# Performance work log

Hardware: AMD Instinct MI355X
Metric: run time of the kernel (lower is better)

Reference implementation:

```python
import jax, jax.numpy as jnp
import numpy as np

D_MODEL = 1024
N_HEADS = 16
N_GROUPS = 4
D_HEAD = D_MODEL // N_HEADS  # 64
HPG = N_HEADS // N_GROUPS    # heads per KV group = 4
B, T = 2, 2048


def _rope(x):
    # x: [B, H, T, D]; interleaved even/odd rotary, matching the torch module
    t, d = x.shape[2], x.shape[3]
    pos = jnp.arange(t, dtype=jnp.float32)[:, None]                      # [T,1]
    freq = jnp.exp(-(jnp.arange(0, d, 2, dtype=jnp.float32) / d)
                   * jnp.log(jnp.float32(10000.0)))                      # [D/2]
    angle = pos * freq                                                   # [T, D/2]
    cos, sin = jnp.cos(angle), jnp.sin(angle)
    xe, xo = x[..., ::2], x[..., 1::2]
    re = xe * cos - xo * sin
    ro = xe * sin + xo * cos
    return jnp.stack([re, ro], axis=-1).reshape(x.shape)


def setup_inputs() -> dict:
    key = jax.random.key(0)
    ks = jax.random.split(key, 10)
    s = 0.02
    return {
        "x":  jax.random.normal(ks[0], (B, T, D_MODEL), dtype=jnp.float32),
        "Wq": jax.random.normal(ks[1], (D_MODEL, D_MODEL), dtype=jnp.float32) * s,
        "bq": jax.random.normal(ks[2], (D_MODEL,), dtype=jnp.float32) * s,
        "Wk": jax.random.normal(ks[3], (D_MODEL, N_GROUPS * D_HEAD), dtype=jnp.float32) * s,
        "bk": jax.random.normal(ks[4], (N_GROUPS * D_HEAD,), dtype=jnp.float32) * s,
        "Wv": jax.random.normal(ks[5], (D_MODEL, N_GROUPS * D_HEAD), dtype=jnp.float32) * s,
        "bv": jax.random.normal(ks[6], (N_GROUPS * D_HEAD,), dtype=jnp.float32) * s,
        "Wo": jax.random.normal(ks[7], (D_MODEL, D_MODEL), dtype=jnp.float32) * s,
        "bo": jax.random.normal(ks[8], (D_MODEL,), dtype=jnp.float32) * s,
    }


def reference(x, Wq, bq, Wk, bk, Wv, bv, Wo, bo):
    b, t, _ = x.shape
    q = (x @ Wq + bq).reshape(b, t, N_HEADS, D_HEAD).transpose(0, 2, 1, 3)    # [B,H,T,D]
    k = (x @ Wk + bk).reshape(b, t, N_GROUPS, D_HEAD).transpose(0, 2, 1, 3)   # [B,G,T,D]
    v = (x @ Wv + bv).reshape(b, t, N_GROUPS, D_HEAD).transpose(0, 2, 1, 3)
    # GQA broadcast: idx = arange(n_heads) // heads_per_group  ==  repeat each group HPG times
    k = jnp.repeat(k, HPG, axis=1)                                            # [B,H,T,D]
    v = jnp.repeat(v, HPG, axis=1)
    q = _rope(q)
    k = _rope(k)
    scale = jnp.float32(np.sqrt(D_HEAD))
    scores = jnp.einsum('bhtd,bhsd->bhts', q, k) / scale                      # [B,H,T,T]
    causal = jnp.tril(jnp.ones((t, t), dtype=bool))
    scores = jnp.where(causal, scores, -jnp.inf)
    probs = jax.nn.softmax(scores, axis=-1)
    # dropout(p=0.05) is identity in eval mode
    attn = jnp.einsum('bhts,bhsd->bhtd', probs, v)
    out = attn.transpose(0, 2, 1, 3).reshape(b, t, N_HEADS * D_HEAD)
    return out @ Wo + bo
```

## Files before the change

kernel.cpp:

```cpp
#include <hip/hip_runtime.h>
#include <stdint.h>

typedef unsigned short u16;
typedef __attribute__((ext_vector_type(4))) float f32x4;
typedef __attribute__((ext_vector_type(8))) short bf16x8;
typedef __attribute__((ext_vector_type(4))) short bf16x4;

#define T_SEQ 2048
#define DM 1024
#define NH 16
#define NG 4
#define DH 64
#define QSCALE 0.18033688011112042f

__device__ __forceinline__ u16 f2bf(float f) {
    union { float f; uint32_t u; } v; v.f = f;
    uint32_t r = (v.u + 0x7FFFu + ((v.u >> 16) & 1u)) >> 16;
    return (u16)r;
}
__device__ __forceinline__ float bf2f(u16 u) {
    union { uint32_t u; float f; } v; v.u = ((uint32_t)u) << 16;
    return v.f;
}
__device__ __forceinline__ float fexp2(float x) {
#if __has_builtin(__builtin_amdgcn_exp2f)
    return __builtin_amdgcn_exp2f(x);
#else
    return exp2f(x);
#endif
}
__device__ __forceinline__ uint32_t cvtpk_bf16(float a, float b) {
    uint32_t r;
    asm("v_cvt_pk_bf16_f32 %0, %1, %2" : "=v"(r) : "v"(a), "v"(b));
    return r;
}

#if __has_builtin(__builtin_amdgcn_mfma_f32_16x16x16_bf16)
__device__ __forceinline__ f32x4 mfma16(bf16x4 a, bf16x4 b, f32x4 c) {
    return __builtin_amdgcn_mfma_f32_16x16x16_bf16(a, b, c, 0, 0, 0);
}
#elif __has_builtin(__builtin_amdgcn_mfma_f32_16x16x16bf16_1k)
__device__ __forceinline__ f32x4 mfma16(bf16x4 a, bf16x4 b, f32x4 c) {
    return __builtin_amdgcn_mfma_f32_16x16x16bf16_1k(a, b, c, 0, 0, 0);
}
#else
__device__ __forceinline__ f32x4 mfma16(bf16x4 a, bf16x4 b, f32x4 c) {
    asm("v_mfma_f32_16x16x16_bf16 %0, %1, %2, %0" : "+v"(c) : "v"(a), "v"(b));
    return c;
}
#endif

__device__ __forceinline__ void async16(const void* g, void* l) {
    __builtin_amdgcn_global_load_lds(
        (const __attribute__((address_space(1))) void*)g,
        (__attribute__((address_space(3))) void*)l,
        16, 0, 0);
}

__global__ __launch_bounds__(256) void k_prep(
    const float* __restrict__ x, u16* __restrict__ xb,
    const float* __restrict__ Wq, const float* __restrict__ Wk,
    const float* __restrict__ Wv, const float* __restrict__ Wo,
    u16* __restrict__ wqkvt, u16* __restrict__ wot,
    const float* __restrict__ bq, const float* __restrict__ bk,
    const float* __restrict__ bv, float* __restrict__ bqkv,
    float2* __restrict__ tbl) {
    int blk = blockIdx.x;
    int tid = threadIdx.x;
    if (blk < 2048) {
        int i = blk * 256 + tid;
        const float4* p = (const float4*)x + (size_t)i * 2;
        float4 a = p[0], b = p[1];
        bf16x8 v;
        v[0] = (short)f2bf(a.x); v[1] = (short)f2bf(a.y);
        v[2] = (short)f2bf(a.z); v[3] = (short)f2bf(a.w);
        v[4] = (short)f2bf(b.x); v[5] = (short)f2bf(b.y);
        v[6] = (short)f2bf(b.z); v[7] = (short)f2bf(b.w);
        ((bf16x8*)xb)[i] = v;
        return;
    }
    int t = blk - 2048;
    if (t >= 2560) {
        int u = t - 2560;
        if (u < 6) {
            int i = u * 256 + tid;
            if (i < 1536) {
                float v;
                if (i < 1024) v = bq[i];
                else if (i < 1280) v = bk[i - 1024];
                else v = bv[i - 1280];
                bqkv[i] = v;
            }
        } else {
            int idx = (u - 6) * 256 + tid;
            int tt = idx >> 5, i = idx & 31;
            float freq = exp2f(-(float)i * (13.287712379549449f / 32.0f));
            float ang = (float)tt * freq;
            tbl[idx] = make_float2(cosf(ang), sinf(ang));
        }
        return;
    }
    const float* src; u16* dst; int N;
    if (t < 1024)      { src = Wq; dst = wqkvt;                      N = 1024; }
    else if (t < 1280) { t -= 1024; src = Wk; dst = wqkvt + (size_t)1024 * 1024; N = 256; }
    else if (t < 1536) { t -= 1280; src = Wv; dst = wqkvt + (size_t)1280 * 1024; N = 256; }
    else               { t -= 1536; src = Wo; dst = wot;             N = 1024; }
    int ntiles = N >> 5;
    int n0 = (t % ntiles) * 32, k0 = (t / ntiles) * 32;
    __shared__ float tile[32][33];
    int tx = tid & 31, ty = tid >> 5;
#pragma unroll
    for (int q = 0; q < 4; q++)
        tile[ty + q * 8][tx] = src[(size_t)(k0 + ty + q * 8) * N + n0 + tx];
    __syncthreads();
#pragma unroll
    for (int q = 0; q < 4; q++)
        dst[(size_t)(n0 + ty + q * 8) * 1024 + k0 + tx] = f2bf(tile[tx][ty + q * 8]);
}

template <int EPI>
__global__ __launch_bounds__(256) void k_gemm(
    const u16* __restrict__ A, const u16* __restrict__ Bt,
    const float* __restrict__ bias, float* __restrict__ C,
    const float2* __restrict__ tbl, u16* __restrict__ Qo,
    u16* __restrict__ Ko, u16* __restrict__ Vto, int N, int K) {
    __shared__ __align__(16) u16 As[2][64 * 64];
    __shared__ __align__(16) u16 Bs[2][128 * 64];
    int tid = threadIdx.x;
    int lane = tid & 63, wid = tid >> 6;
    int wr = wid >> 1, wc = wid & 1;
    int l15 = lane & 15, lhi = lane >> 4;
    int row0 = blockIdx.y * 64, col0 = blockIdx.x * 128;
    f32x4 acc[2][4] = {};

    const u16* ga[2];
    const u16* gb[4];
#pragma unroll
    for (int i = 0; i < 2; i++) {
        int c = i * 256 + tid, r = c >> 3, sch = (c & 7) ^ (r & 7);
        ga[i] = A + (size_t)(row0 + r) * K + sch * 8;
    }
#pragma unroll
    for (int i = 0; i < 4; i++) {
        int c = i * 256 + tid, r = c >> 3, sch = (c & 7) ^ (r & 7);
        gb[i] = Bt + (size_t)(col0 + r) * K + sch * 8;
    }

#pragma unroll
    for (int i = 0; i < 2; i++) async16(ga[i], &As[0][(i * 256 + tid) * 8]);
#pragma unroll
    for (int i = 0; i < 4; i++) async16(gb[i], &Bs[0][(i * 256 + tid) * 8]);
    __syncthreads();

    int nk = K >> 6;
    for (int kt = 0; kt < nk; kt++) {
        int cur = kt & 1;
        if (kt + 1 < nk) {
            int nx = cur ^ 1, ko = (kt + 1) << 6;
#pragma unroll
            for (int i = 0; i < 2; i++) async16(ga[i] + ko, &As[nx][(i * 256 + tid) * 8]);
#pragma unroll
            for (int i = 0; i < 4; i++) async16(gb[i] + ko, &Bs[nx][(i * 256 + tid) * 8]);
        }
        const u16* Ac = As[cur];
        const u16* Bc = Bs[cur];
#pragma unroll
        for (int ks = 0; ks < 2; ks++) {
            bf16x8 af[2], bfr[4];
#pragma unroll
            for (int m = 0; m < 2; m++) {
                int r = wr * 32 + m * 16 + l15;
                int kb = (ks * 64 + lhi * 16) ^ ((r & 7) << 4);
                af[m] = *(const bf16x8*)((const char*)Ac + r * 128 + kb);
            }
#pragma unroll
            for (int n = 0; n < 4; n++) {
                int r = wc * 64 + n * 16 + l15;
                int kb = (ks * 64 + lhi * 16) ^ ((r & 7) << 4);
                bfr[n] = *(const bf16x8*)((const char*)Bc + r * 128 + kb);
            }
#pragma unroll
            for (int m = 0; m < 2; m++)
#pragma unroll
                for (int n = 0; n < 4; n++)
                    acc[m][n] = __builtin_amdgcn_mfma_f32_16x16x32_bf16(
                        af[m], bfr[n], acc[m][n], 0, 0, 0);
        }
        __syncthreads();
    }

    if (EPI == 0) {
#pragma unroll
        for (int n = 0; n < 4; n++) {
            int col = col0 + wc * 64 + n * 16 + l15;
            float bv = bias[col];
#pragma unroll
            for (int m = 0; m < 2; m++) {
                int row = row0 + wr * 32 + m * 16 + lhi * 4;
#pragma unroll
                for (int i = 0; i < 4; i++)
                    C[(size_t)(row + i) * N + col] = acc[m][n][i] + bv;
            }
        }
    } else {
        int type = (col0 >= 1280) ? 2 : (col0 >= 1024 ? 1 : 0);
        int rbase = row0 + wr * 32;
#pragma unroll
        for (int n = 0; n < 4; n++) {
            int col = col0 + wc * 64 + n * 16 + l15;
            float bv = bias[col];
            if (type == 2) {
                int cc = col - 1280;
                int g = cc >> 6, d = cc & 63;
#pragma unroll
                for (int m = 0; m < 2; m++)
#pragma unroll
                    for (int i = 0; i < 4; i++) {
                        int rowg = rbase + m * 16 + lhi * 4 + i;
                        int t = rowg & (T_SEQ - 1), b = rowg >> 11;
                        int sp = t ^ ((d & 1) << 2);
                        Vto[(((size_t)(b * NG + g)) * DH + d) * T_SEQ + sp] =
                            f2bf(acc[m][n][i] + bv);
                    }
            } else {
                float ssgn = (col & 1) ? 1.f : -1.f;
                int ip = (col & 63) >> 1;
#pragma unroll
                for (int m = 0; m < 2; m++)
#pragma unroll
                    for (int i = 0; i < 4; i++) {
                        int rowg = rbase + m * 16 + lhi * 4 + i;
                        int t = rowg & (T_SEQ - 1), b = rowg >> 11;
                        float v = acc[m][n][i] + bv;
                        float other = __shfl_xor(v, 1);
                        float2 cs = tbl[t * 32 + ip];
                        float out = v * cs.x + other * cs.y * ssgn;
                        if (type == 0) {
                            int h = col >> 6, d = col & 63;
                            Qo[(((size_t)(b * NH + h)) * T_SEQ + t) * DH + d] =
                                f2bf(out * QSCALE);
                        } else {
                            int cc = col - 1024;
                            int g = cc >> 6, d = cc & 63;
                            Ko[(((size_t)(b * NG + g)) * T_SEQ + t) * DH + d] = f2bf(out);
                        }
                    }
            }
        }
    }
}

__global__ __launch_bounds__(256) void k_attn(
    const u16* __restrict__ Q, const u16* __restrict__ K,
    const u16* __restrict__ Vt, u16* __restrict__ Aout) {
    int i0 = blockIdx.x;
    int u = i0 >> 5;
    int qt = (u < 16) ? (31 - u) : (u - 16);
    int bh = i0 & 31;
    int b = bh >> 4, h = bh & 15, g = h >> 2;
    int tid = threadIdx.x;
    int lane = tid & 63, wid = tid >> 6;
    int l15 = lane & 15, lhi = lane >> 4;

    const u16* Kp = K + ((size_t)(b * NG + g)) * T_SEQ * DH;
    const u16* Vp = Vt + ((size_t)(b * NG + g)) * DH * T_SEQ;

    __shared__ __align__(16) u16 Ks[2][64 * 64];
    __shared__ __align__(16) u16 Vs[3][64 * 64];

    const u16* Qp = Q + ((size_t)bh * T_SEQ + qt * 64) * DH;
    bf16x8 qf[2];
#pragma unroll
    for (int ks = 0; ks < 2; ks++)
        qf[ks] = *(const bf16x8*)(Qp + (size_t)(wid * 16 + l15) * DH + ks * 32 + lhi * 8);

    f32x4 of[4] = {};
    float m_i = -3.0e38f, l_i = 0.f;

    int nt = qt + 1;
    int swz = (l15 & 7) << 4;

    int c0 = tid, c1 = tid + 256;
    int rk0 = c0 >> 3, rk1 = c1 >> 3;
    int sk0 = (c0 & 7) ^ (rk0 & 7);
    int sk1 = (c1 & 7) ^ (rk1 & 7);
    int sv0 = (c0 & 7) ^ ((rk0 >> 1) & 7);
    int sv1 = (c1 & 7) ^ ((rk1 >> 1) & 7);
    const u16* kg0 = Kp + rk0 * DH + sk0 * 8;
    const u16* kg1 = Kp + rk1 * DH + sk1 * 8;
    const u16* vg0 = Vp + (size_t)rk0 * T_SEQ + sv0 * 8;
    const u16* vg1 = Vp + (size_t)rk1 * T_SEQ + sv1 * 8;

    async16(kg0, &Ks[0][c0 * 8]);
    async16(kg1, &Ks[0][c1 * 8]);
    async16(vg0, &Vs[0][c0 * 8]);
    async16(vg1, &Vs[0][c1 * 8]);
    __syncthreads();
    if (nt > 1) {
        async16(kg0 + (1 << 12), &Ks[1][c0 * 8]);
        async16(kg1 + (1 << 12), &Ks[1][c1 * 8]);
        async16(vg0 + (1 << 6), &Vs[1][c0 * 8]);
        async16(vg1 + (1 << 6), &Vs[1][c1 * 8]);
    }
    f32x4 sf[4] = {};
    __builtin_amdgcn_s_setprio(1);
#pragma unroll
    for (int ks = 0; ks < 2; ks++)
#pragma unroll
        for (int n = 0; n < 4; n++) {
            int kb = (ks * 64 + lhi * 16) ^ swz;
            bf16x8 kf = *(const bf16x8*)((const char*)Ks[0] + (n * 16 + l15) * 128 + kb);
            sf[n] = __builtin_amdgcn_mfma_f32_16x16x32_bf16(kf, qf[ks], sf[n], 0, 0, 0);
        }
    __builtin_amdgcn_s_setprio(0);
    __syncthreads();

    u16* vread = Vs[0];
    u16* vhold = Vs[1];
    u16* vstage = Vs[2];

#pragma unroll 1
    for (int it = 1; it < nt; it++) {
        if (it + 1 < nt) {
            int ko = (it + 1) << 12, vo = (it + 1) << 6;
            int nx = (it + 1) & 1;
            async16(kg0 + ko, &Ks[nx][c0 * 8]);
            async16(kg1 + ko, &Ks[nx][c1 * 8]);
            async16(vg0 + vo, vstage + c0 * 8);
            async16(vg1 + vo, vstage + c1 * 8);
        }

        float pmt = sf[0][0];
#pragma unroll
        for (int n = 0; n < 4; n++)
#pragma unroll
            for (int i = 0; i < 4; i++)
                pmt = fmaxf(pmt, sf[n][i]);
        if (!__all(pmt - m_i <= 8.f)) {
#pragma unroll
            for (int off = 16; off <= 32; off <<= 1)
                pmt = fmaxf(pmt, __shfl_xor(pmt, off));
            float mn = fmaxf(m_i, pmt);
            float sc = fexp2(m_i - mn);
            m_i = mn;
            l_i *= sc;
            float sc4[4];
#pragma unroll
            for (int i = 0; i < 4; i++)
                sc4[i] = __shfl(sc, lhi * 4 + i);
#pragma unroll
            for (int n = 0; n < 4; n++)
#pragma unroll
                for (int i = 0; i < 4; i++)
                    of[n][i] *= sc4[i];
        }
        bf16x4 pa[4];
#pragma unroll
        for (int n = 0; n < 4; n++) {
#pragma unroll
            for (int i = 0; i < 4; i++) {
                float p = fexp2(sf[n][i] - m_i);
                sf[n][i] = p;
                l_i += p;
            }
            union { uint32_t uu[2]; bf16x4 v; } pu;
            pu.uu[0] = cvtpk_bf16(sf[n][0], sf[n][1]);
            pu.uu[1] = cvtpk_bf16(sf[n][2], sf[n][3]);
            pa[n] = pu.v;
        }

        const u16* Kc = Ks[it & 1];
        __builtin_amdgcn_s_setprio(1);
#pragma unroll
        for (int ks = 0; ks < 2; ks++)
#pragma unroll
            for (int n = 0; n < 4; n++) {
                int kb = (ks * 64 + lhi * 16) ^ swz;
                bf16x8 kf = *(const bf16x8*)((const char*)Kc + (n * 16 + l15) * 128 + kb);
                f32x4 z = (ks == 0) ? f32x4{0.f, 0.f, 0.f, 0.f} : sf[n];
                sf[n] = __builtin_amdgcn_mfma_f32_16x16x32_bf16(kf, qf[ks], z, 0, 0, 0);
            }

#pragma unroll
        for (int nd = 0; nd < 4; nd++) {
            int rowb = (nd * 16 + l15) * 128;
#pragma unroll
            for (int n = 0; n < 4; n++) {
                int kb = ((4 * n + lhi) ^ l15) << 3;
                bf16x4 vf = *(const bf16x4*)((const char*)vread + rowb + kb);
                of[nd] = mfma16(pa[n], vf, of[nd]);
            }
        }
        __builtin_amdgcn_s_setprio(0);

        u16* tmp = vread; vread = vhold; vhold = vstage; vstage = tmp;
        __syncthreads();
    }

    {
        int qrow = qt * 64 + wid * 16 + l15;
        int sb = (nt - 1) * 64 + lhi * 4;
#pragma unroll
        for (int n = 0; n < 4; n++)
#pragma unroll
            for (int i = 0; i < 4; i++)
                if (sb + n * 16 + i > qrow) sf[n][i] = -3.0e38f;
        float pmt = sf[0][0];
#pragma unroll
        for (int n = 0; n < 4; n++)
#pragma unroll
            for (int i = 0; i < 4; i++)
                pmt = fmaxf(pmt, sf[n][i]);
        if (!__all(pmt - m_i <= 8.f)) {
#pragma unroll
            for (int off = 16; off <= 32; off <<= 1)
                pmt = fmaxf(pmt, __shfl_xor(pmt, off));
            float mn = fmaxf(m_i, pmt);
            float sc = fexp2(m_i - mn);
            m_i = mn;
            l_i *= sc;
            float sc4[4];
#pragma unroll
            for (int i = 0; i < 4; i++)
                sc4[i] = __shfl(sc, lhi * 4 + i);
#pragma unroll
            for (int n = 0; n < 4; n++)
#pragma unroll
                for (int i = 0; i < 4; i++)
                    of[n][i] *= sc4[i];
        }
        bf16x4 pa[4];
#pragma unroll
        for (int n = 0; n < 4; n++) {
#pragma unroll
            for (int i = 0; i < 4; i++) {
                float p = fexp2(sf[n][i] - m_i);
                sf[n][i] = p;
                l_i += p;
            }
            union { uint32_t uu[2]; bf16x4 v; } pu;
            pu.uu[0] = cvtpk_bf16(sf[n][0], sf[n][1]);
            pu.uu[1] = cvtpk_bf16(sf[n][2], sf[n][3]);
            pa[n] = pu.v;
        }
        __builtin_amdgcn_s_setprio(1);
#pragma unroll
        for (int nd = 0; nd < 4; nd++) {
            int rowb = (nd * 16 + l15) * 128;
#pragma unroll
            for (int n = 0; n < 4; n++) {
                int kb = ((4 * n + lhi) ^ l15) << 3;
                bf16x4 vf = *(const bf16x4*)((const char*)vread + rowb + kb);
                of[nd] = mfma16(pa[n], vf, of[nd]);
            }
        }
        __builtin_amdgcn_s_setprio(0);
    }

#pragma unroll
    for (int off = 16; off <= 32; off <<= 1)
        l_i += __shfl_xor(l_i, off);
    float lq[4];
#pragma unroll
    for (int i = 0; i < 4; i++)
        lq[i] = __shfl(l_i, lhi * 4 + i);
#pragma unroll
    for (int n = 0; n < 4; n++)
#pragma unroll
        for (int i = 0; i < 4; i++) {
            int trow = qt * 64 + wid * 16 + lhi * 4 + i;
            float v = of[n][i] / lq[i];
            Aout[((size_t)(b * T_SEQ + trow)) * DM + h * 64 + n * 16 + l15] = f2bf(v);
        }
}

extern "C" void kernel_launch(void* const* d_in, const int* in_sizes, int n_in,
                              void* d_out, int out_size, void* d_ws, size_t ws_size,
                              hipStream_t stream) {
    const float* x  = (const float*)d_in[0];
    const float* Wq = (const float*)d_in[1];
    const float* bq = (const float*)d_in[2];
    const float* Wk = (const float*)d_in[3];
    const float* bk = (const float*)d_in[4];
    const float* Wv = (const float*)d_in[5];
    const float* bv = (const float*)d_in[6];
    const float* Wo = (const float*)d_in[7];
    const float* bo = (const float*)d_in[8];

    char* ws = (char*)d_ws;
    size_t o = 0;
    u16*   xb    = (u16*)(ws + o);  o += (size_t)4096 * 1024 * 2;
    u16*   wqkvt = (u16*)(ws + o);  o += (size_t)1536 * 1024 * 2;
    u16*   wot   = (u16*)(ws + o);  o += (size_t)1024 * 1024 * 2;
    float* bqkv  = (float*)(ws + o); o += 1536 * 4;
    o = (o + 255) & ~(size_t)255;
    u16*   Qb    = (u16*)(ws + o);  o += (size_t)2 * NH * T_SEQ * DH * 2;
    u16*   Kb    = (u16*)(ws + o);  o += (size_t)2 * NG * T_SEQ * DH * 2;
    u16*   Vtb   = (u16*)(ws + o);  o += (size_t)2 * NG * DH * T_SEQ * 2;
    u16*   attnb = (u16*)(ws + o);  o += (size_t)4096 * 1024 * 2;
    float2* tbl  = (float2*)(ws + o); o += (size_t)2048 * 32 * 8;

    k_prep<<<4870, 256, 0, stream>>>(x, xb, Wq, Wk, Wv, Wo, wqkvt, wot, bq, bk, bv, bqkv, tbl);
    k_gemm<1><<<dim3(12, 64), 256, 0, stream>>>(xb, wqkvt, bqkv, nullptr, tbl, Qb, Kb, Vtb, 1536, 1024);
    k_attn<<<1024, 256, 0, stream>>>(Qb, Kb, Vtb, attnb);
    k_gemm<0><<<dim3(8, 64), 256, 0, stream>>>(attnb, wot, bo, (float*)d_out, nullptr, nullptr, nullptr, nullptr, 1024, 1024);
}
```

Baseline: 88.58 us.

## Shrink GEMM column tiles and fold running max into attention score accumulator

The GEMM kernels get a template parameter for the column tile width. The QKV projection now uses 96-wide tiles and the output projection 64-wide tiles, which raises block counts to fill more CUs at the cost of less B-operand reuse. In attention, the running max is subtracted by seeding the QK MFMA accumulator with -m_i, so the common no-rescale path computes exp2 directly without a subtract. The 16-way max reduction also uses v_max3. This adds a duplicated exp path, and it changes initial m_i to 0, which relies on the threshold logic staying numerically safe.

Result: slower. 91.41 us (+3.2%).

```diff
diff --git a/kernel.cpp b/kernel.cpp
--- a/kernel.cpp
+++ b/kernel.cpp
@@ -32,6 +32,11 @@
 __device__ __forceinline__ uint32_t cvtpk_bf16(float a, float b) {
     uint32_t r;
     asm("v_cvt_pk_bf16_f32 %0, %1, %2" : "=v"(r) : "v"(a), "v"(b));
+    return r;
+}
+__device__ __forceinline__ float max3f(float a, float b, float c) {
+    float r;
+    asm("v_max3_f32 %0, %1, %2, %3" : "=v"(r) : "v"(a), "v"(b), "v"(c));
     return r;
 }
 
@@ -118,30 +123,30 @@
         dst[(size_t)(n0 + ty + q * 8) * 1024 + k0 + tx] = f2bf(tile[tx][ty + q * 8]);
 }
 
-template <int EPI>
+template <int EPI, int NB>
 __global__ __launch_bounds__(256) void k_gemm(
     const u16* __restrict__ A, const u16* __restrict__ Bt,
     const float* __restrict__ bias, float* __restrict__ C,
     const float2* __restrict__ tbl, u16* __restrict__ Qo,
     u16* __restrict__ Ko, u16* __restrict__ Vto, int N, int K) {
     __shared__ __align__(16) u16 As[2][64 * 64];
-    __shared__ __align__(16) u16 Bs[2][128 * 64];
+    __shared__ __align__(16) u16 Bs[2][NB * 32 * 64];
     int tid = threadIdx.x;
     int lane = tid & 63, wid = tid >> 6;
     int wr = wid >> 1, wc = wid & 1;
     int l15 = lane & 15, lhi = lane >> 4;
-    int row0 = blockIdx.y * 64, col0 = blockIdx.x * 128;
-    f32x4 acc[2][4] = {};
+    int row0 = blockIdx.y * 64, col0 = blockIdx.x * (NB * 32);
+    f32x4 acc[2][NB] = {};
 
     const u16* ga[2];
-    const u16* gb[4];
+    const u16* gb[NB];
 #pragma unroll
     for (int i = 0; i < 2; i++) {
         int c = i * 256 + tid, r = c >> 3, sch = (c & 7) ^ (r & 7);
         ga[i] = A + (size_t)(row0 + r) * K + sch * 8;
     }
 #pragma unroll
-    for (int i = 0; i < 4; i++) {
+    for (int i = 0; i < NB; i++) {
         int c = i * 256 + tid, r = c >> 3, sch = (c & 7) ^ (r & 7);
         gb[i] = Bt + (size_t)(col0 + r) * K + sch * 8;
     }
@@ -149,7 +154,7 @@
 #pragma unroll
     for (int i = 0; i < 2; i++) async16(ga[i], &As[0][(i * 256 + tid) * 8]);
 #pragma unroll
-    for (int i = 0; i < 4; i++) async16(gb[i], &Bs[0][(i * 256 + tid) * 8]);
+    for (int i = 0; i < NB; i++) async16(gb[i], &Bs[0][(i * 256 + tid) * 8]);
     __syncthreads();
 
     int nk = K >> 6;
@@ -160,13 +165,13 @@
 #pragma unroll
             for (int i = 0; i < 2; i++) async16(ga[i] + ko, &As[nx][(i * 256 + tid) * 8]);
 #pragma unroll
-            for (int i = 0; i < 4; i++) async16(gb[i] + ko, &Bs[nx][(i * 256 + tid) * 8]);
+            for (int i = 0; i < NB; i++) async16(gb[i] + ko, &Bs[nx][(i * 256 + tid) * 8]);
         }
         const u16* Ac = As[cur];
         const u16* Bc = Bs[cur];
 #pragma unroll
         for (int ks = 0; ks < 2; ks++) {
-            bf16x8 af[2], bfr[4];
+            bf16x8 af[2], bfr[NB];
 #pragma unroll
             for (int m = 0; m < 2; m++) {
                 int r = wr * 32 + m * 16 + l15;
@@ -174,78 +179,70 @@
                 af[m] = *(const bf16x8*)((const char*)Ac + r * 128 + kb);
             }
 #pragma unroll
-            for (int n = 0; n < 4; n++) {
-                int r = wc * 64 + n * 16 + l15;
+            for (int n = 0; n < NB; n++) {
+                int r = wc * (NB * 16) + n * 16 + l15;
                 int kb = (ks * 64 + lhi * 16) ^ ((r & 7) << 4);
                 bfr[n] = *(const bf16x8*)((const char*)Bc + r * 128 + kb);
             }
 #pragma unroll
             for (int m = 0; m < 2; m++)
 #pragma unroll
-                for (int n = 0; n < 4; n++)
+                for (int n = 0; n < NB; n++)
                     acc[m][n] = __builtin_amdgcn_mfma_f32_16x16x32_bf16(
                         af[m], bfr[n], acc[m][n], 0, 0, 0);
         }
         __syncthreads();
     }
 
-    if (EPI == 0) {
-#pragma unroll
-        for (int n = 0; n < 4; n++) {
-            int col = col0 + wc * 64 + n * 16 + l15;
-            float bv = bias[col];
+    int rbase = row0 + wr * 32;
+#pragma unroll
+    for (int n = 0; n < NB; n++) {
+        int col = col0 + wc * (NB * 16) + n * 16 + l15;
+        float bv = bias[col];
+        if (EPI == 0) {
 #pragma unroll
             for (int m = 0; m < 2; m++) {
-                int row = row0 + wr * 32 + m * 16 + lhi * 4;
+                int row = rbase + m * 16 + lhi * 4;
 #pragma unroll
                 for (int i = 0; i < 4; i++)
                     C[(size_t)(row + i) * N + col] = acc[m][n][i] + bv;
             }
-        }
-    } else {
-        int type = (col0 >= 1280) ? 2 : (col0 >= 1024 ? 1 : 0);
-        int rbase = row0 + wr * 32;
-#pragma unroll
-        for (int n = 0; n < 4; n++) {
-            int col = col0 + wc * 64 + n * 16 + l15;
-            float bv = bias[col];
-            if (type == 2) {
-                int cc = col - 1280;
-                int g = cc >> 6, d = cc & 63;
-#pragma unroll
-                for (int m = 0; m < 2; m++)
-#pragma unroll
-                    for (int i = 0; i < 4; i++) {
-                        int rowg = rbase + m * 16 + lhi * 4 + i;
-                        int t = rowg & (T_SEQ - 1), b = rowg >> 11;
-                        int sp = t ^ ((d & 1) << 2);
-                        Vto[(((size_t)(b * NG + g)) * DH + d) * T_SEQ + sp] =
-                            f2bf(acc[m][n][i] + bv);
+        } else if (col >= 1280) {
+            int cc = col - 1280;
+            int g = cc >> 6, d = cc & 63;
+#pragma unroll
+            for (int m = 0; m < 2; m++)
+#pragma unroll
+                for (int i = 0; i < 4; i++) {
+                    int rowg = rbase + m * 16 + lhi * 4 + i;
+                    int t = rowg & (T_SEQ - 1), b = rowg >> 11;
+                    int sp = t ^ ((d & 1) << 2);
+                    Vto[(((size_t)(b * NG + g)) * DH + d) * T_SEQ + sp] =
+                        f2bf(acc[m][n][i] + bv);
+                }
+        } else {
+            float ssgn = (col & 1) ? 1.f : -1.f;
+            int ip = (col & 63) >> 1;
+#pragma unroll
+            for (int m = 0; m < 2; m++)
+#pragma unroll
+                for (int i = 0; i < 4; i++) {
+                    int rowg = rbase + m * 16 + lhi * 4 + i;
+                    int t = rowg & (T_SEQ - 1), b = rowg >> 11;
+                    float v = acc[m][n][i] + bv;
+                    float other = __shfl_xor(v, 1);
+                    float2 cs = tbl[t * 32 + ip];
+                    float out = v * cs.x + other * cs.y * ssgn;
+                    if (col < 1024) {
+                        int h = col >> 6, d = col & 63;
+                        Qo[(((size_t)(b * NH + h)) * T_SEQ + t) * DH + d] =
+                            f2bf(out * QSCALE);
+                    } else {
+                        int cc = col - 1024;
+                        int g = cc >> 6, d = cc & 63;
+                        Ko[(((size_t)(b * NG + g)) * T_SEQ + t) * DH + d] = f2bf(out);
                     }
-            } else {
-                float ssgn = (col & 1) ? 1.f : -1.f;
-                int ip = (col & 63) >> 1;
-#pragma unroll
-                for (int m = 0; m < 2; m++)
-#pragma unroll
-                    for (int i = 0; i < 4; i++) {
-                        int rowg = rbase + m * 16 + lhi * 4 + i;
-                        int t = rowg & (T_SEQ - 1), b = rowg >> 11;
-                        float v = acc[m][n][i] + bv;
-                        float other = __shfl_xor(v, 1);
-                        float2 cs = tbl[t * 32 + ip];
-                        float out = v * cs.x + other * cs.y * ssgn;
-                        if (type == 0) {
-                            int h = col >> 6, d = col & 63;
-                            Qo[(((size_t)(b * NH + h)) * T_SEQ + t) * DH + d] =
-                                f2bf(out * QSCALE);
-                        } else {
-                            int cc = col - 1024;
-                            int g = cc >> 6, d = cc & 63;
-                            Ko[(((size_t)(b * NG + g)) * T_SEQ + t) * DH + d] = f2bf(out);
-                        }
-                    }
-            }
+                }
         }
     }
 }
@@ -275,7 +272,7 @@
         qf[ks] = *(const bf16x8*)(Qp + (size_t)(wid * 16 + l15) * DH + ks * 32 + lhi * 8);
 
     f32x4 of[4] = {};
-    float m_i = -3.0e38f, l_i = 0.f;
+    float m_i = 0.f, l_i = 0.f;
 
     int nt = qt + 1;
     int swz = (l15 & 7) << 4;
@@ -330,19 +327,20 @@
             async16(vg1 + vo, vstage + c1 * 8);
         }
 
-        float pmt = sf[0][0];
-#pragma unroll
-        for (int n = 0; n < 4; n++)
-#pragma unroll
-            for (int i = 0; i < 4; i++)
-                pmt = fmaxf(pmt, sf[n][i]);
-        if (!__all(pmt - m_i <= 8.f)) {
+        float t0 = max3f(sf[0][0], sf[0][1], sf[0][2]);
+        float t1 = max3f(sf[0][3], sf[1][0], sf[1][1]);
+        float t2 = max3f(sf[1][2], sf[1][3], sf[2][0]);
+        float t3 = max3f(sf[2][1], sf[2][2], sf[2][3]);
+        float t4 = max3f(sf[3][0], sf[3][1], sf[3][2]);
+        float pmt = fmaxf(max3f(t0, t1, t2), max3f(t3, t4, sf[3][3]));
+        bf16x4 pa[4];
+        if (!__all(pmt <= 8.f)) {
 #pragma unroll
             for (int off = 16; off <= 32; off <<= 1)
                 pmt = fmaxf(pmt, __shfl_xor(pmt, off));
-            float mn = fmaxf(m_i, pmt);
-            float sc = fexp2(m_i - mn);
-            m_i = mn;
+            float dm = fmaxf(pmt, 0.f);
+            m_i += dm;
+            float sc = fexp2(-dm);
             l_i *= sc;
             float sc4[4];
 #pragma unroll
@@ -353,22 +351,36 @@
 #pragma unroll
                 for (int i = 0; i < 4; i++)
                     of[n][i] *= sc4[i];
-        }
-        bf16x4 pa[4];
-#pragma unroll
-        for (int n = 0; n < 4; n++) {
-#pragma unroll
-            for (int i = 0; i < 4; i++) {
-                float p = fexp2(sf[n][i] - m_i);
-                sf[n][i] = p;
-                l_i += p;
-            }
-            union { uint32_t uu[2]; bf16x4 v; } pu;
-            pu.uu[0] = cvtpk_bf16(sf[n][0], sf[n][1]);
-            pu.uu[1] = cvtpk_bf16(sf[n][2], sf[n][3]);
-            pa[n] = pu.v;
-        }
-
+#pragma unroll
+            for (int n = 0; n < 4; n++) {
+#pragma unroll
+                for (int i = 0; i < 4; i++) {
+                    float p = fexp2(sf[n][i] - dm);
+                    sf[n][i] = p;
+                    l_i += p;
+                }
+                union { uint32_t uu[2]; bf16x4 v; } pu;
+                pu.uu[0] = cvtpk_bf16(sf[n][0], sf[n][1]);
+                pu.uu[1] = cvtpk_bf16(sf[n][2], sf[n][3]);
+                pa[n] = pu.v;
+            }
+        } else {
+#pragma unroll
+            for (int n = 0; n < 4; n++) {
+#pragma unroll
+                for (int i = 0; i < 4; i++) {
+                    float p = fexp2(sf[n][i]);
+                    sf[n][i] = p;
+                    l_i += p;
+                }
+                union { uint32_t uu[2]; bf16x4 v; } pu;
+                pu.uu[0] = cvtpk_bf16(sf[n][0], sf[n][1]);
+                pu.uu[1] = cvtpk_bf16(sf[n][2], sf[n][3]);
+                pa[n] = pu.v;
+            }
+        }
+
+        float nm = -m_i;
         const u16* Kc = Ks[it & 1];
         __builtin_amdgcn_s_setprio(1);
 #pragma unroll
@@ -377,7 +389,7 @@
             for (int n = 0; n < 4; n++) {
                 int kb = (ks * 64 + lhi * 16) ^ swz;
                 bf16x8 kf = *(const bf16x8*)((const char*)Kc + (n * 16 + l15) * 128 + kb);
-                f32x4 z = (ks == 0) ? f32x4{0.f, 0.f, 0.f, 0.f} : sf[n];
+                f32x4 z = (ks == 0) ? f32x4{nm, nm, nm, nm} : sf[n];
                 sf[n] = __builtin_amdgcn_mfma_f32_16x16x32_bf16(kf, qf[ks], z, 0, 0, 0);
             }
 
@@ -405,19 +417,19 @@
 #pragma unroll
             for (int i = 0; i < 4; i++)
                 if (sb + n * 16 + i > qrow) sf[n][i] = -3.0e38f;
-        float pmt = sf[0][0];
-#pragma unroll
-        for (int n = 0; n < 4; n++)
-#pragma unroll
-            for (int i = 0; i < 4; i++)
-                pmt = fmaxf(pmt, sf[n][i]);
-        if (!__all(pmt - m_i <= 8.f)) {
+        float t0 = max3f(sf[0][0], sf[0][1], sf[0][2]);
+        float t1 = max3f(sf[0][3], sf[1][0], sf[1][1]);
+        float t2 = max3f(sf[1][2], sf[1][3], sf[2][0]);
+        float t3 = max3f(sf[2][1], sf[2][2], sf[2][3]);
+        float t4 = max3f(sf[3][0], sf[3][1], sf[3][2]);
+        float pmt = fmaxf(max3f(t0, t1, t2), max3f(t3, t4, sf[3][3]));
+        bf16x4 pa[4];
+        if (!__all(pmt <= 8.f)) {
 #pragma unroll
             for (int off = 16; off <= 32; off <<= 1)
                 pmt = fmaxf(pmt, __shfl_xor(pmt, off));
-            float mn = fmaxf(m_i, pmt);
-            float sc = fexp2(m_i - mn);
-            m_i = mn;
+            float dm = fmaxf(pmt, 0.f);
+            float sc = fexp2(-dm);
             l_i *= sc;
             float sc4[4];
 #pragma unroll
@@ -428,20 +440,33 @@
 #pragma unroll
                 for (int i = 0; i < 4; i++)
                     of[n][i] *= sc4[i];
-        }
-        bf16x4 pa[4];
-#pragma unroll
-        for (int n = 0; n < 4; n++) {
-#pragma unroll
-            for (int i = 0; i < 4; i++) {
-                float p = fexp2(sf[n][i] - m_i);
-                sf[n][i] = p;
-                l_i += p;
-            }
-            union { uint32_t uu[2]; bf16x4 v; } pu;
-            pu.uu[0] = cvtpk_bf16(sf[n][0], sf[n][1]);
-            pu.uu[1] = cvtpk_bf16(sf[n][2], sf[n][3]);
-            pa[n] = pu.v;
+#pragma unroll
+            for (int n = 0; n < 4; n++) {
+#pragma unroll
+                for (int i = 0; i < 4; i++) {
+                    float p = fexp2(sf[n][i] - dm);
+                    sf[n][i] = p;
+                    l_i += p;
+                }
+                union { uint32_t uu[2]; bf16x4 v; } pu;
+                pu.uu[0] = cvtpk_bf16(sf[n][0], sf[n][1]);
+                pu.uu[1] = cvtpk_bf16(sf[n][2], sf[n][3]);
+                pa[n] = pu.v;
+            }
+        } else {
+#pragma unroll
+            for (int n = 0; n < 4; n++) {
+#pragma unroll
+                for (int i = 0; i < 4; i++) {
+                    float p = fexp2(sf[n][i]);
+                    sf[n][i] = p;
+                    l_i += p;
+                }
+                union { uint32_t uu[2]; bf16x4 v; } pu;
+                pu.uu[0] = cvtpk_bf16(sf[n][0], sf[n][1]);
+                pu.uu[1] = cvtpk_bf16(sf[n][2], sf[n][3]);
+                pa[n] = pu.v;
+            }
         }
         __builtin_amdgcn_s_setprio(1);
 #pragma unroll
@@ -501,7 +526,7 @@
     float2* tbl  = (float2*)(ws + o); o += (size_t)2048 * 32 * 8;
 
     k_prep<<<4870, 256, 0, stream>>>(x, xb, Wq, Wk, Wv, Wo, wqkvt, wot, bq, bk, bv, bqkv, tbl);
-    k_gemm<1><<<dim3(12, 64), 256, 0, stream>>>(xb, wqkvt, bqkv, nullptr, tbl, Qb, Kb, Vtb, 1536, 1024);
+    k_gemm<1, 3><<<dim3(16, 64), 256, 0, stream>>>(xb, wqkvt, bqkv, nullptr, tbl, Qb, Kb, Vtb, 1536, 1024);
     k_attn<<<1024, 256, 0, stream>>>(Qb, Kb, Vtb, attnb);
-    k_gemm<0><<<dim3(8, 64), 256, 0, stream>>>(attnb, wot, bo, (float*)d_out, nullptr, nullptr, nullptr, nullptr, 1024, 1024);
-}
+    k_gemm<0, 2><<<dim3(16, 64), 256, 0, stream>>>(attnb, wot, bo, (float*)d_out, nullptr, nullptr, nullptr, nullptr, 1024, 1024);
+}
```

## Split long causal query tiles across two blocks with a combine kernel

Applied to the files above, without the earlier changes.

Query tiles 16-31, which carry the most causal KV work, are each split into two blocks that cover halves of the KV range. The halves write unnormalized partial outputs plus row max and sum to workspace, and a new combine kernel merges them with a log-sum-exp rescale. A constant task table interleaves split and unsplit work to even out load across the 1536 blocks. The goal is to shorten the critical path of the longest blocks, at the cost of an extra kernel launch and fp32 partial-output traffic.

Result: slower. 92.25 us (+4.1%).

```diff
diff --git a/kernel.cpp b/kernel.cpp
--- a/kernel.cpp
+++ b/kernel.cpp
@@ -56,6 +56,15 @@
         (__attribute__((address_space(3))) void*)l,
         16, 0, 0);
 }
+
+__constant__ unsigned char d_task_qt[48] = {
+    31,31,30,15,30,29,29,28,14,28,27,27,26,13,26,25,25,24,12,24,
+    23,23,22,11,22,21,21,20,10,20,19,19,18, 9,18,17,17,16, 8,16,
+     7, 6, 5, 4, 3, 2, 1, 0};
+__constant__ unsigned char d_task_sh[48] = {
+    2,3,2,0,3,2,3,2,0,3,2,3,2,0,3,2,3,2,0,3,
+    2,3,2,0,3,2,3,2,0,3,2,3,2,0,3,2,3,2,0,3,
+    0,0,0,0,0,0,0,0};
 
 __global__ __launch_bounds__(256) void k_prep(
     const float* __restrict__ x, u16* __restrict__ xb,
@@ -252,11 +261,19 @@
 
 __global__ __launch_bounds__(256) void k_attn(
     const u16* __restrict__ Q, const u16* __restrict__ K,
-    const u16* __restrict__ Vt, u16* __restrict__ Aout) {
-    int i0 = blockIdx.x;
-    int u = i0 >> 5;
-    int qt = (u < 16) ? (31 - u) : (u - 16);
-    int bh = i0 & 31;
+    const u16* __restrict__ Vt, u16* __restrict__ Aout,
+    float* __restrict__ Opart, float* __restrict__ mlbuf) {
+    int w = blockIdx.x >> 5;
+    int bh = blockIdx.x & 31;
+    int qt = d_task_qt[w];
+    int sh = d_task_sh[w];
+    int split = sh >> 1, half = sh & 1;
+    int hmid = (qt + 2) >> 1;
+    int t0 = (split && half) ? hmid : 0;
+    int t1 = split ? (half ? qt + 1 : hmid) : qt + 1;
+    int nt = t1 - t0;
+    int diag = (t1 == qt + 1);
+
     int b = bh >> 4, h = bh & 15, g = h >> 2;
     int tid = threadIdx.x;
     int lane = tid & 63, wid = tid >> 6;
@@ -276,8 +293,6 @@
 
     f32x4 of[4] = {};
     float m_i = -3.0e38f, l_i = 0.f;
-
-    int nt = qt + 1;
     int swz = (l15 & 7) << 4;
 
     int c0 = tid, c1 = tid + 256;
@@ -291,16 +306,20 @@
     const u16* vg0 = Vp + (size_t)rk0 * T_SEQ + sv0 * 8;
     const u16* vg1 = Vp + (size_t)rk1 * T_SEQ + sv1 * 8;
 
-    async16(kg0, &Ks[0][c0 * 8]);
-    async16(kg1, &Ks[0][c1 * 8]);
-    async16(vg0, &Vs[0][c0 * 8]);
-    async16(vg1, &Vs[0][c1 * 8]);
+    {
+        int ko = t0 << 12, vo = t0 << 6;
+        async16(kg0 + ko, &Ks[0][c0 * 8]);
+        async16(kg1 + ko, &Ks[0][c1 * 8]);
+        async16(vg0 + vo, &Vs[0][c0 * 8]);
+        async16(vg1 + vo, &Vs[0][c1 * 8]);
+    }
     __syncthreads();
     if (nt > 1) {
-        async16(kg0 + (1 << 12), &Ks[1][c0 * 8]);
-        async16(kg1 + (1 << 12), &Ks[1][c1 * 8]);
-        async16(vg0 + (1 << 6), &Vs[1][c0 * 8]);
-        async16(vg1 + (1 << 6), &Vs[1][c1 * 8]);
+        int ko = (t0 + 1) << 12, vo = (t0 + 1) << 6;
+        async16(kg0 + ko, &Ks[1][c0 * 8]);
+        async16(kg1 + ko, &Ks[1][c1 * 8]);
+        async16(vg0 + vo, &Vs[1][c0 * 8]);
+        async16(vg1 + vo, &Vs[1][c1 * 8]);
     }
     f32x4 sf[4] = {};
     __builtin_amdgcn_s_setprio(1);
@@ -322,7 +341,7 @@
 #pragma unroll 1
     for (int it = 1; it < nt; it++) {
         if (it + 1 < nt) {
-            int ko = (it + 1) << 12, vo = (it + 1) << 6;
+            int ko = (t0 + it + 1) << 12, vo = (t0 + it + 1) << 6;
             int nx = (it + 1) & 1;
             async16(kg0 + ko, &Ks[nx][c0 * 8]);
             async16(kg1 + ko, &Ks[nx][c1 * 8]);
@@ -398,13 +417,15 @@
     }
 
     {
-        int qrow = qt * 64 + wid * 16 + l15;
-        int sb = (nt - 1) * 64 + lhi * 4;
-#pragma unroll
-        for (int n = 0; n < 4; n++)
-#pragma unroll
-            for (int i = 0; i < 4; i++)
-                if (sb + n * 16 + i > qrow) sf[n][i] = -3.0e38f;
+        if (diag) {
+            int qrow = qt * 64 + wid * 16 + l15;
+            int sb = (t1 - 1) * 64 + lhi * 4;
+#pragma unroll
+            for (int n = 0; n < 4; n++)
+#pragma unroll
+                for (int i = 0; i < 4; i++)
+                    if (sb + n * 16 + i > qrow) sf[n][i] = -3.0e38f;
+        }
         float pmt = sf[0][0];
 #pragma unroll
         for (int n = 0; n < 4; n++)
@@ -460,18 +481,68 @@
 #pragma unroll
     for (int off = 16; off <= 32; off <<= 1)
         l_i += __shfl_xor(l_i, off);
-    float lq[4];
-#pragma unroll
-    for (int i = 0; i < 4; i++)
-        lq[i] = __shfl(l_i, lhi * 4 + i);
-#pragma unroll
-    for (int n = 0; n < 4; n++)
-#pragma unroll
-        for (int i = 0; i < 4; i++) {
-            int trow = qt * 64 + wid * 16 + lhi * 4 + i;
-            float v = of[n][i] / lq[i];
-            Aout[((size_t)(b * T_SEQ + trow)) * DM + h * 64 + n * 16 + l15] = f2bf(v);
-        }
+
+    if (split) {
+        int tileix = (qt - 16) * 32 + bh;
+        float* Op = Opart + ((size_t)tileix * 2 + half) * 4096;
+#pragma unroll
+        for (int n = 0; n < 4; n++)
+#pragma unroll
+            for (int i = 0; i < 4; i++)
+                Op[(wid * 16 + lhi * 4 + i) * 64 + n * 16 + l15] = of[n][i];
+        if (lhi == 0) {
+            int base = tileix * 256 + half * 128;
+            mlbuf[base + wid * 16 + l15] = m_i;
+            mlbuf[base + 64 + wid * 16 + l15] = l_i;
+        }
+    } else {
+        float lq[4];
+#pragma unroll
+        for (int i = 0; i < 4; i++)
+            lq[i] = __shfl(l_i, lhi * 4 + i);
+#pragma unroll
+        for (int n = 0; n < 4; n++)
+#pragma unroll
+            for (int i = 0; i < 4; i++) {
+                int trow = qt * 64 + wid * 16 + lhi * 4 + i;
+                float v = of[n][i] / lq[i];
+                Aout[((size_t)(b * T_SEQ + trow)) * DM + h * 64 + n * 16 + l15] = f2bf(v);
+            }
+    }
+}
+
+__global__ __launch_bounds__(256) void k_combine(
+    const float* __restrict__ Opart, const float* __restrict__ mlbuf,
+    u16* __restrict__ Aout) {
+    int j = blockIdx.x;
+    int qt = 16 + (j >> 5), bh = j & 31;
+    int b = bh >> 4, h = bh & 15;
+    int tid = threadIdx.x;
+    int lane = tid & 63, wid = tid >> 6;
+    int l15 = lane & 15, lhi = lane >> 4;
+
+    const float* OA = Opart + (size_t)j * 2 * 4096;
+    const float* OB = OA + 4096;
+    int mb = j * 256;
+
+#pragma unroll
+    for (int i = 0; i < 4; i++) {
+        int r = wid * 16 + lhi * 4 + i;
+        float mA = mlbuf[mb + r];
+        float lA = mlbuf[mb + 64 + r];
+        float mB = mlbuf[mb + 128 + r];
+        float lB = mlbuf[mb + 192 + r];
+        float M = fmaxf(mA, mB);
+        float sA = fexp2(mA - M), sB = fexp2(mB - M);
+        float linv = 1.f / (lA * sA + lB * sB);
+        int trow = qt * 64 + r;
+#pragma unroll
+        for (int n = 0; n < 4; n++) {
+            int d = n * 16 + l15;
+            float v = (OA[r * 64 + d] * sA + OB[r * 64 + d] * sB) * linv;
+            Aout[((size_t)(b * T_SEQ + trow)) * DM + h * 64 + d] = f2bf(v);
+        }
+    }
 }
 
 extern "C" void kernel_launch(void* const* d_in, const int* in_sizes, int n_in,
@@ -499,9 +570,12 @@
     u16*   Vtb   = (u16*)(ws + o);  o += (size_t)2 * NG * DH * T_SEQ * 2;
     u16*   attnb = (u16*)(ws + o);  o += (size_t)4096 * 1024 * 2;
     float2* tbl  = (float2*)(ws + o); o += (size_t)2048 * 32 * 8;
+    float* Opart = (float*)(ws + o); o += (size_t)512 * 2 * 4096 * 4;
+    float* mlbuf = (float*)(ws + o); o += (size_t)512 * 256 * 4;
 
     k_prep<<<4870, 256, 0, stream>>>(x, xb, Wq, Wk, Wv, Wo, wqkvt, wot, bq, bk, bv, bqkv, tbl);
     k_gemm<1><<<dim3(12, 64), 256, 0, stream>>>(xb, wqkvt, bqkv, nullptr, tbl, Qb, Kb, Vtb, 1536, 1024);
-    k_attn<<<1024, 256, 0, stream>>>(Qb, Kb, Vtb, attnb);
+    k_attn<<<1536, 256, 0, stream>>>(Qb, Kb, Vtb, attnb, Opart, mlbuf);
+    k_combine<<<512, 256, 0, stream>>>(Opart, mlbuf, attnb);
     k_gemm<0><<<dim3(8, 64), 256, 0, stream>>>(attnb, wot, bo, (float*)d_out, nullptr, nullptr, nullptr, nullptr, 1024, 1024);
 }
```
